# Optimization experiments

Hardware: AMD Instinct MI355X
Metric: run time of the kernel (lower is better)

Reference implementation:

```python
import jax, jax.numpy as jnp
import numpy as np

DEPTH = 4  # init kwarg 'depth'
H = 256   # init kwarg 'hidden_size'
ATOM_FDIM, BOND_FDIM = 35, 5


def _build_graph(rng, N, E):
    src = rng.integers(0, N, E).astype(np.int32)
    dst = rng.integers(0, N, E).astype(np.int32)
    # line graph (backtracking=False): lg edge e1 -> e2 iff dst[e1]==src[e2] and src[e1]!=dst[e2]
    indeg = np.bincount(dst, minlength=N)
    idx_sorted = np.argsort(dst, kind='stable')          # edge ids grouped by dst node
    ptr = np.concatenate([[0], np.cumsum(indeg)]).astype(np.int64)
    counts = indeg[src]                                   # in-edges of src[e] feed edge e
    total = int(counts.sum())
    lg_dst = np.repeat(np.arange(E, dtype=np.int64), counts)
    cum = np.cumsum(counts) - counts
    within = np.arange(total) - np.repeat(cum, counts)
    lg_src = idx_sorted[np.repeat(ptr[src], counts) + within]
    keep = src[lg_src] != dst[lg_dst]                     # drop backtracking pairs
    return src, dst, lg_src[keep].astype(np.int32), lg_dst[keep].astype(np.int32)


def setup_inputs() -> dict:
    rng = np.random.default_rng(0)
    N, E, Et, K, G = 50000, 200000, 100000, 50000, 2000
    src, dst, lg_src, lg_dst = _build_graph(rng, N, E)
    graph_ids = ((np.arange(N, dtype=np.int64) * G) // N).astype(np.int32)
    f32 = lambda *s: rng.standard_normal(s).astype(np.float32)
    return {
        'x_nodes': jnp.asarray(f32(N, ATOM_FDIM)),
        'x_edges': jnp.asarray(rng.random((E, BOND_FDIM)).astype(np.float32)),
        'tree_m': jnp.asarray(f32(Et, H) * 0.1),
        'W_i': jnp.asarray(f32(ATOM_FDIM + BOND_FDIM, H) * 0.05),
        'W_h': jnp.asarray(f32(H, H) * 0.05),
        'W_o': jnp.asarray(f32(ATOM_FDIM + H, H) * 0.05),
        'b_o': jnp.asarray(f32(H) * 0.05),
        'edge_src': jnp.asarray(src),
        'edge_dst': jnp.asarray(dst),
        'lg_src': jnp.asarray(lg_src),
        'lg_dst': jnp.asarray(lg_dst),
        'tgt_nodes': jnp.asarray(rng.integers(0, N, K).astype(np.int32)),
        'tree_eid': jnp.asarray(rng.integers(0, Et, K).astype(np.int32)),
        'graph_ids': jnp.asarray(graph_ids),
        'n_graphs': G,
    }


def reference(x_nodes, x_edges, tree_m, W_i, W_h, W_o, b_o,
              edge_src, edge_dst, lg_src, lg_dst, tgt_nodes, tree_eid,
              graph_ids, n_graphs):
    N = x_nodes.shape[0]
    E = x_edges.shape[0]
    # edge input features: [src atom feats | bond feats] @ W_i (no bias)
    msg_input = jnp.concatenate([x_nodes[edge_src], x_edges], axis=1) @ W_i  # [E,H]
    msg = jax.nn.relu(msg_input)
    # tree message alignment: scatter-add tree edge messages onto cand nodes
    node_alpha = jnp.zeros((N, msg.shape[1]), msg.dtype).at[tgt_nodes].add(tree_m[tree_eid])
    edge_alpha = node_alpha[edge_src]  # apply_edges: alpha = src alpha
    # loopy BP over the line graph
    for _ in range(DEPTH - 1):
        accum = jax.ops.segment_sum(msg[lg_src], lg_dst, num_segments=E)  # [E,H]
        msg = jax.nn.relu(msg_input + (accum + edge_alpha) @ W_h)
    # gather: m = sum of incoming edge messages per node
    m = jax.ops.segment_sum(msg, edge_dst, num_segments=N)  # [N,H]
    h = jax.nn.relu(jnp.concatenate([x_nodes, m + node_alpha], axis=1) @ W_o + b_o)
    # mean_nodes per candidate graph
    sums = jax.ops.segment_sum(h, graph_ids, num_segments=n_graphs)
    cnt = jax.ops.segment_sum(jnp.ones((N, 1), h.dtype), graph_ids, num_segments=n_graphs)
    return sums / jnp.maximum(cnt, 1.0)
```

## Files before the change

### kernel.cpp

```cpp
#include <hip/hip_runtime.h>
#include <stdint.h>

typedef unsigned short u16;
typedef __attribute__((ext_vector_type(8))) short bf16x8;
typedef __attribute__((ext_vector_type(4))) float f32x4;

#define HD 256
#define AST 264
#define CORR_CAP 2048

static __device__ __forceinline__ float b2f(u16 x){
  union{float f; unsigned u;} v; v.u = ((unsigned)x)<<16; return v.f;
}
static __device__ __forceinline__ u16 f2b(float f){
  union{float f; unsigned u;} v; v.f = f;
  unsigned r = v.u + 0x7fffu + ((v.u>>16)&1u);
  return (u16)(r>>16);
}
static __device__ __forceinline__ void racc2(float* a, uint2 iv, uint2 vv){
  float t0 = b2f((u16)iv.x)       + b2f((u16)vv.x);
  float t1 = b2f((u16)(iv.x>>16)) + b2f((u16)(vv.x>>16));
  float t2 = b2f((u16)iv.y)       + b2f((u16)vv.y);
  float t3 = b2f((u16)(iv.y>>16)) + b2f((u16)(vv.y>>16));
  a[0] += t0>0.f?t0:0.f; a[1] += t1>0.f?t1:0.f;
  a[2] += t2>0.f?t2:0.f; a[3] += t3>0.f?t3:0.f;
}
static __device__ __forceinline__ void racc1(float* a, uint2 iv){
  float t0 = b2f((u16)iv.x), t1 = b2f((u16)(iv.x>>16));
  float t2 = b2f((u16)iv.y), t3 = b2f((u16)(iv.y>>16));
  a[0] += t0>0.f?t0:0.f; a[1] += t1>0.f?t1:0.f;
  a[2] += t2>0.f?t2:0.f; a[3] += t3>0.f?t3:0.f;
}

__global__ void k_zero_int(int* __restrict__ p, int n){
  int i = blockIdx.x*256 + threadIdx.x;
  if (i < n) p[i] = 0;
}

__global__ void k_hist(const int* __restrict__ key, int* __restrict__ deg, int n){
  int i = blockIdx.x*256 + threadIdx.x;
  if (i < n) atomicAdd(&deg[key[i]], 1);
}

__global__ void k_scan_p1(const int* __restrict__ deg, int n, int* __restrict__ bsum){
  int i = blockIdx.x*256 + threadIdx.x;
  int v = (i < n) ? deg[i] : 0;
  #pragma unroll
  for (int o=32; o>0; o>>=1) v += __shfl_down(v, o);
  __shared__ int w[4];
  if ((threadIdx.x&63)==0) w[threadIdx.x>>6] = v;
  __syncthreads();
  if (threadIdx.x==0) bsum[blockIdx.x] = w[0]+w[1]+w[2]+w[3];
}
__global__ __launch_bounds__(1024) void k_scan_p2(int* __restrict__ bsum, int nb,
                                                  int* __restrict__ total_dst){
  __shared__ int sm[1024];
// ... 14 lines not shown
  int t = threadIdx.x;
  int i = blockIdx.x*256 + t;
  int v = (i < n) ? deg[i] : 0;
  __shared__ int sm[256];
  sm[t] = v; __syncthreads();
  for (int o=1; o<256; o<<=1){
    int u = (t>=o) ? sm[t-o] : 0;
    __syncthreads();
    sm[t] += u;
    __syncthreads();
  }
  int ex = sm[t] - v + bsum[blockIdx.x];
  if (i < n){ start[i] = ex; cursor[i] = ex; }
}

__global__ void k_fill(const int* __restrict__ key, const int* __restrict__ val,
                       int* __restrict__ cursor, int* __restrict__ bucket, int n){
  int i = blockIdx.x*256 + threadIdx.x;
  if (i >= n) return;
  int pos = atomicAdd(&cursor[key[i]], 1);
  bucket[pos] = val ? val[i] : i;
}

__global__ void k_permarr(const int* __restrict__ perm, const int* __restrict__ esrc,
                          const int* __restrict__ edst, int* __restrict__ esrc_p,
                          int* __restrict__ edst_p, int E){
  int e = blockIdx.x*256 + threadIdx.x;
  if (e >= E) return;
  int o = perm[e];
  esrc_p[e] = esrc[o];
  edst_p[e] = edst[o];
}

__global__ void k_xep(const float* __restrict__ xe, const int* __restrict__ perm,
                      float* __restrict__ xep, int E){
  int e = blockIdx.x*256 + threadIdx.x;
  if (e >= E) return;
  int o = perm[e];
  #pragma unroll
  for (int k=0;k<5;k++) xep[(size_t)e*5+k] = xe[(size_t)o*5+k];
}

__global__ void k_xnf(const float* __restrict__ xn, u16* __restrict__ xnf, int N){
  int g = blockIdx.x*256 + threadIdx.x;
  int v2 = g >> 6, c = g & 63;
  if (v2 >= N) return;
  float v = (c < 35) ? xn[(size_t)v2*35 + c] : 0.f;
  xnf[g] = f2b(v);
}

__global__ void k_alpha_gather(const float* __restrict__ tree_m, const int* __restrict__ start,
                               const int* __restrict__ bucket, u16* __restrict__ alpha16, int N){
  int v = (int)(((long long)blockIdx.x*blockDim.x + threadIdx.x)>>6);
  int l = threadIdx.x & 63;
  if (v >= N) return;
  int s = start[v], e2 = start[v+1];
  float a0=0.f,a1=0.f,a2=0.f,a3=0.f;
  for (int j=s;j<e2;j++){
    float4 tv = *(const float4*)(tree_m + (size_t)bucket[j]*HD + l*4);
    a0 += tv.x; a1 += tv.y; a2 += tv.z; a3 += tv.w;
  }
  ushort4 o; o.x=f2b(a0); o.y=f2b(a1); o.z=f2b(a2); o.w=f2b(a3);
  *(ushort4*)(alpha16 + (size_t)v*HD + l*4) = o;
}

__global__ void k_prep_frag(const float* __restrict__ W, int k0, int kmax, int nks,
                            u16* __restrict__ out){
  int g = blockIdx.x*256 + threadIdx.x;
  if (g >= nks*16*512) return;
  int i = g & 7, l = (g>>3)&63, t = g>>9;
  int nj = t & 15, ks = t >> 4;
  int n = nj*16 + (l&15);
  int k = ks*32 + (l>>4)*8 + i;
  float v = (k < kmax) ? W[(size_t)(k0+k)*HD + n] : 0.f;
  out[g] = f2b(v);
}

__global__ __launch_bounds__(512, 4) void k_pr_gemm(
    const u16* __restrict__ featA, const u16* __restrict__ BTf,
    u16* __restrict__ out16, int M)
{
  const int tid = threadIdx.x;
  const int w = tid>>6, l = tid&63;
  const int lr = l&15, lq = l>>4;
  const int nrb = (M+15)>>4;
  bf16x8 B0[2], B1[2];
  #pragma unroll
  for (int ks=0; ks<2; ks++){
    B0[ks] = *(const bf16x8*)(BTf + (size_t)((ks*16 + w*2  )*512) + l*8);
    B1[ks] = *(const bf16x8*)(BTf + (size_t)((ks*16 + w*2+1)*512) + l*8);
  }
  const int c0 = w*32 + lr, c1 = w*32 + 16 + lr;
  for (int rb = blockIdx.x; rb < nrb; rb += gridDim.x){
    int r = rb*16 + lr; int rc = min(r, M-1);
    const u16* fr = featA + (size_t)rc*64 + lq*8;
    bf16x8 a0 = *(const bf16x8*)(fr);
    bf16x8 a1 = *(const bf16x8*)(fr + 32);
    f32x4 acc0 = (f32x4){0.f,0.f,0.f,0.f};
    f32x4 acc1 = (f32x4){0.f,0.f,0.f,0.f};
    acc0 = __builtin_amdgcn_mfma_f32_16x16x32_bf16(a0, B0[0], acc0, 0,0,0);
    acc0 = __builtin_amdgcn_mfma_f32_16x16x32_bf16(a1, B0[1], acc0, 0,0,0);
    acc1 = __builtin_amdgcn_mfma_f32_16x16x32_bf16(a0, B1[0], acc1, 0,0,0);
    acc1 = __builtin_amdgcn_mfma_f32_16x16x32_bf16(a1, B1[1], acc1, 0,0,0);
    #pragma unroll
    for (int reg=0; reg<4; reg++){
      int gm = rb*16 + lq*4 + reg;
      if (gm < M){
        out16[(size_t)gm*HD + c0] = f2b(acc0[reg]);
        out16[(size_t)gm*HD + c1] = f2b(acc1[reg]);
      }
    }
  }
}

__global__ __launch_bounds__(256, 8) void k_build_I(
    const u16* __restrict__ P, const float* __restrict__ xep,
    const int* __restrict__ esrc_p, const float* __restrict__ Wi,
    u16* __restrict__ I, int E)
{
  const int l = threadIdx.x & 63;
  const int wid = (blockIdx.x*256 + threadIdx.x) >> 6;
  const int nw = gridDim.x*4;
  float wq[5][4];
  #pragma unroll
// ... 4 lines not shown
  for (int e = wid; e < E; e += nw){
    int s = esrc_p[e];
    const float* xp = xep + (size_t)e*5;
    float x0=xp[0], x1=xp[1], x2=xp[2], x3=xp[3], x4=xp[4];
    uint2 uv = *(const uint2*)(P + (size_t)s*HD + l*4);
    float v[4] = { b2f((u16)uv.x), b2f((u16)(uv.x>>16)),
                   b2f((u16)uv.y), b2f((u16)(uv.y>>16)) };
    #pragma unroll
    for (int j=0;j<4;j++)
      v[j] += x0*wq[0][j] + x1*wq[1][j] + x2*wq[2][j] + x3*wq[3][j] + x4*wq[4][j];
    ushort4 o; o.x=f2b(v[0]); o.y=f2b(v[1]); o.z=f2b(v[2]); o.w=f2b(v[3]);
    *(ushort4*)(I + (size_t)e*HD + l*4) = o;
  }
}

__global__ void k_pairs(const int* __restrict__ esrc_p, const int* __restrict__ edst_p,
                        const int* __restrict__ start_d,
                        int* __restrict__ npairs, int2* __restrict__ pairs, int E){
  int e = blockIdx.x*256 + threadIdx.x;
  if (e >= E) return;
  int u = esrc_p[e], v = edst_p[e];
  int s = start_d[u], t = start_d[u+1];
  for (int ep=s; ep<t; ep++){
    if (esrc_p[ep] == v){
      int pos = atomicAdd(npairs, 1);
      if (pos < CORR_CAP) pairs[pos] = (int2){e, ep};
    }
  }
}

__global__ void k_msgA0(const u16* __restrict__ I, const int2* __restrict__ pairs,
                        const int* __restrict__ npairs_p, float* __restrict__ msgA){
  int np = *npairs_p; if (np > CORR_CAP) np = CORR_CAP;
  int t = threadIdx.x;
  for (int p = blockIdx.x; p < np; p += gridDim.x){
    int ep = pairs[p].y;
    float v = b2f(I[(size_t)ep*HD + t]);
    msgA[(size_t)p*HD + t] = v > 0.f ? v : 0.f;
  }
}

__global__ __launch_bounds__(512, 4) void k_bp(
    const u16* __restrict__ I, const u16* __restrict__ Vprev,
    const u16* __restrict__ alpha16, const int* __restrict__ start_d,
    const int* __restrict__ esrc_p, const u16* __restrict__ BTf,
    const u16* __restrict__ Radd, const float* __restrict__ bias,
    u16* __restrict__ Sout, u16* __restrict__ Vout, float* __restrict__ hout,
    int N, int mode)
{
  __shared__ u16 A_lds[16][AST];
  const int tid = threadIdx.x;
  const int w = tid>>6, l = tid&63;
  const int lr = l&15, lq = l>>4;
  const int ngrp = (N+15)>>4;

  bf16x8 B0[8], B1[8];
  #pragma unroll
  for (int ks=0; ks<8; ks++){
    B0[ks] = *(const bf16x8*)(BTf + (size_t)((ks*16 + w*2  )*512) + l*8);
    B1[ks] = *(const bf16x8*)(BTf + (size_t)((ks*16 + w*2+1)*512) + l*8);
  }
  const int c0 = w*32 + lr, c1 = w*32 + 16 + lr;
  float b0 = 0.f, b1 = 0.f;
  if (mode == 1){ b0 = bias[c0]; b1 = bias[c1]; }

  for (int grp = blockIdx.x; grp < ngrp; grp += gridDim.x){
    const int vb = grp*16;
    #pragma unroll
    for (int hh=0; hh<2; hh++){
      int v = vb + w*2 + hh;
      float a[4] = {0.f,0.f,0.f,0.f};
      if (v < N){
        uint2 av = *(const uint2*)(alpha16 + (size_t)v*HD + l*4);
        a[0]=b2f((u16)av.x); a[1]=b2f((u16)(av.x>>16));
        a[2]=b2f((u16)av.y); a[3]=b2f((u16)(av.y>>16));
        int s = start_d[v], e2 = start_d[v+1];
        int cnt = e2 - s;
        const u16* Ir = I + (size_t)s*HD + l*4;
        if (Vprev){
          const int* sp = esrc_p + s;
          int j = 0;
          for (; j+2 <= cnt; j+=2){
            int s0 = sp[j], s1 = sp[j+1];
            uint2 i0 = *(const uint2*)(Ir);
            uint2 i1 = *(const uint2*)(Ir + HD);
            uint2 v0 = *(const uint2*)(Vprev + (size_t)s0*HD + l*4);
            uint2 v1 = *(const uint2*)(Vprev + (size_t)s1*HD + l*4);
            Ir += 2*HD;
            racc2(a, i0, v0); racc2(a, i1, v1);
          }
          if (j < cnt){
            int s0 = sp[j];
            uint2 i0 = *(const uint2*)(Ir);
            uint2 v0 = *(const uint2*)(Vprev + (size_t)s0*HD + l*4);
            racc2(a, i0, v0);
          }
        } else {
          int j = 0;
          for (; j+2 <= cnt; j+=2){
            uint2 i0 = *(const uint2*)(Ir);
            uint2 i1 = *(const uint2*)(Ir + HD);
            Ir += 2*HD;
            racc1(a, i0); racc1(a, i1);
          }
          if (j < cnt) racc1(a, *(const uint2*)(Ir));
        }
      }
      ushort4 o; o.x=f2b(a[0]); o.y=f2b(a[1]); o.z=f2b(a[2]); o.w=f2b(a[3]);
      if (v < N) *(ushort4*)(Sout + (size_t)v*HD + l*4) = o;
      *(ushort4*)&A_lds[w*2+hh][l*4] = o;
    }
    __syncthreads();
    f32x4 acc0 = (f32x4){0.f,0.f,0.f,0.f};
    f32x4 acc1 = (f32x4){0.f,0.f,0.f,0.f};
    const u16* Ar = &A_lds[lr][0];
    #pragma unroll
    for (int ks=0; ks<8; ks++){
      bf16x8 af = *(const bf16x8*)(Ar + ks*32 + lq*8);
      acc0 = __builtin_amdgcn_mfma_f32_16x16x32_bf16(af, B0[ks], acc0, 0,0,0);
      acc1 = __builtin_amdgcn_mfma_f32_16x16x32_bf16(af, B1[ks], acc1, 0,0,0);
    }
    #pragma unroll
    for (int reg=0; reg<4; reg++){
      int gm = vb + lq*4 + reg;
      if (gm < N){
        if (mode == 1){
          float v0 = acc0[reg] + b2f(Radd[(size_t)gm*HD + c0]) + b0;
          float v1 = acc1[reg] + b2f(Radd[(size_t)gm*HD + c1]) + b1;
          hout[(size_t)gm*HD + c0] = v0 > 0.f ? v0 : 0.f;
          hout[(size_t)gm*HD + c1] = v1 > 0.f ? v1 : 0.f;
        } else {
          Vout[(size_t)gm*HD + c0] = f2b(acc0[reg]);
          Vout[(size_t)gm*HD + c1] = f2b(acc1[reg]);
        }
      }
    }
    __syncthreads();
  }
}

__global__ __launch_bounds__(256) void k_corr1(
    const u16* __restrict__ I, const u16* __restrict__ Vprev,
    const int* __restrict__ esrc_p,
    const int2* __restrict__ pairs, const int* __restrict__ npairs_p,
    const float* __restrict__ Wh, const float* __restrict__ msgA,
    float* __restrict__ newA, float* __restrict__ deltaS)
{
  int np = *npairs_p; if (np > CORR_CAP) np = CORR_CAP;
// ... 14 lines not shown
      float a0=0.f,a1=0.f,a2=0.f,a3=0.f;
      for (int k=0;k<HD;k+=4){
        a0 += cs[k]  *Wh[(size_t)k*HD+t];
        a1 += cs[k+1]*Wh[(size_t)(k+1)*HD+t];
        a2 += cs[k+2]*Wh[(size_t)(k+2)*HD+t];
        a3 += cs[k+3]*Wh[(size_t)(k+3)*HD+t];
      }
      float corr = (a0+a1)+(a2+a3);
      int u = esrc_p[e];
      float base = b2f(I[(size_t)e*HD + t]) + b2f(Vprev[(size_t)u*HD + t]);
      float mn = base > 0.f ? base : 0.f;
      float bt = base - corr;
      float mt = bt > 0.f ? bt : 0.f;
      deltaS[(size_t)p*HD + t] = mt - mn;
      for (int q=0;q<np;q++) if (pairs[q].y == e) newA[(size_t)q*HD + t] = mt;
    }
  }
}

__global__ __launch_bounds__(256, 1) void k_corr2(
    const int2* __restrict__ pairs, const int* __restrict__ npairs_p,
    const int* __restrict__ edst_p, const float* __restrict__ deltaS,
    float* __restrict__ msgA, const float* __restrict__ newA,
    u16* __restrict__ Scur)
{
  int np = *npairs_p; if (np > CORR_CAP) np = CORR_CAP;
  int t = threadIdx.x;
  for (int p=0; p<np; p++){
    msgA[(size_t)p*HD + t] = newA[(size_t)p*HD + t];
    int e = pairs[p].x;
    bool first = true;
    for (int q=0;q<p;q++) if (pairs[q].x == e){ first=false; break; }
    if (first){
      int dv = edst_p[e];
      u16* sp = Scur + (size_t)dv*HD + t;
      *sp = f2b(b2f(*sp) + deltaS[(size_t)p*HD + t]);
    }
    __syncthreads();
  }
}

__global__ __launch_bounds__(256) void k_corr3(
    const int2* __restrict__ pairs, const int* __restrict__ npairs_p,
    const int* __restrict__ edst_p, const u16* __restrict__ Scur,
    const float* __restrict__ Wh, const float* __restrict__ Wob,
    const u16* __restrict__ Radd, const float* __restrict__ bias,
    u16* __restrict__ Vcur, float* __restrict__ hout, int isfinal)
{
  int np = *npairs_p; if (np > CORR_CAP) np = CORR_CAP;
  int t = threadIdx.x;
  __shared__ float sa[HD];
  for (int p = blockIdx.x; p < np; p += gridDim.x){
    int dv = edst_p[pairs[p].x];
    bool first = true;
    for (int q=0;q<p;q++) if (edst_p[pairs[q].x] == dv){ first=false; break; }
    __syncthreads();
    if (first) sa[t] = b2f(Scur[(size_t)dv*HD + t]);
    __syncthreads();
    if (first){
      const float* W = isfinal ? Wob : Wh;
      float a0=0.f,a1=0.f,a2=0.f,a3=0.f;
      for (int k=0;k<HD;k+=4){
        a0 += sa[k]  *W[(size_t)k*HD+t];
        a1 += sa[k+1]*W[(size_t)(k+1)*HD+t];
        a2 += sa[k+2]*W[(size_t)(k+2)*HD+t];
        a3 += sa[k+3]*W[(size_t)(k+3)*HD+t];
      }
      float acc = (a0+a1)+(a2+a3);
      if (isfinal){
        float hv = acc + b2f(Radd[(size_t)dv*HD + t]) + bias[t];
        hout[(size_t)dv*HD + t] = hv > 0.f ? hv : 0.f;
      } else {
        Vcur[(size_t)dv*HD + t] = f2b(acc);
      }
    }
  }
}

__global__ void k_graph_mean(const float* __restrict__ h, const int* __restrict__ gid,
                             int N, int G, float* __restrict__ out){
  int g = (int)(((long long)blockIdx.x*blockDim.x + threadIdx.x)>>6);
  int l = threadIdx.x & 63;
  if (g >= G) return;
  int lo=0, hi=N;
  while (lo<hi){ int mid=(lo+hi)>>1; if (gid[mid] < g) lo=mid+1; else hi=mid; }
  int b = lo;
  hi = N;
  while (lo<hi){ int mid=(lo+hi)>>1; if (gid[mid] < g+1) lo=mid+1; else hi=mid; }
  int e2 = lo;
// ... 16 lines not shown
  const float* tree_m  = (const float*)d_in[2];
  const float* W_i     = (const float*)d_in[3];
  const float* W_h     = (const float*)d_in[4];
  const float* W_o     = (const float*)d_in[5];
  const float* b_o     = (const float*)d_in[6];
  const int* edge_src = (const int*)d_in[7];
  const int* edge_dst = (const int*)d_in[8];
  const int* tgt      = (const int*)d_in[11];
  const int* teid     = (const int*)d_in[12];
  const int* gid      = (const int*)d_in[13];

  const int N = in_sizes[0]/35;
  const int E = in_sizes[1]/5;
  const int K = in_sizes[11];
  const int G = out_size/HD;

  char* wsb = (char*)d_ws;
  auto align256 = [](size_t x){ return (x + 255) & ~(size_t)255; };
  size_t oI      = 0;
  size_t oSa     = oI      + align256((size_t)E*HD*2);
  size_t oVa     = oSa     + align256((size_t)N*HD*2);
  size_t oP      = oVa     + align256((size_t)N*HD*2);
  size_t oVb     = oP      + align256((size_t)N*HD*2);
  size_t oR      = oVb     + align256((size_t)N*HD*2);
  size_t oAlpha  = oR      + align256((size_t)N*HD*2);
  size_t oXnf    = oAlpha  + align256((size_t)N*HD*2);
  size_t oXep    = oXnf    + align256((size_t)N*64*2);
  size_t oBTP    = oXep    + align256((size_t)E*5*4);
  size_t oBTWh   = oBTP    + align256((size_t)2*16*512*2);
  size_t oBTRa   = oBTWh   + align256((size_t)8*16*512*2);
  size_t oBTWob  = oBTRa   + align256((size_t)2*16*512*2);
  size_t oDegD   = oBTWob  + align256((size_t)8*16*512*2);
  size_t oStartD = oDegD   + align256((size_t)(N+1)*4);
  size_t oCurD   = oStartD + align256((size_t)(N+1)*4);
  size_t oPerm   = oCurD   + align256((size_t)N*4);
  size_t oEsrcP  = oPerm   + align256((size_t)E*4);
  size_t oEdstP  = oEsrcP  + align256((size_t)E*4);
  size_t oDegT   = oEdstP  + align256((size_t)E*4);
  size_t oStartT = oDegT   + align256((size_t)N*4);
  size_t oCurT   = oStartT + align256((size_t)(N+1)*4);
  size_t oBukT   = oCurT   + align256((size_t)N*4);
  size_t oBsum   = oBukT   + align256((size_t)K*4);
  size_t oPairs  = oBsum   + align256((size_t)1024*4);
  size_t oMsgA   = oPairs  + align256((size_t)CORR_CAP*8);
  size_t oNewA   = oMsgA   + align256((size_t)CORR_CAP*HD*4);
  size_t oDeltaS = oNewA   + align256((size_t)CORR_CAP*HD*4);

  u16*   I       = (u16*)(wsb + oI);
  u16*   Sa      = (u16*)(wsb + oSa);
  u16*   Va      = (u16*)(wsb + oVa);
  u16*   P       = (u16*)(wsb + oP);
  u16*   Vb      = (u16*)(wsb + oVb);
  u16*   R       = (u16*)(wsb + oR);
  u16*   alpha16 = (u16*)(wsb + oAlpha);
  u16*   xnf     = (u16*)(wsb + oXnf);
  float* xep     = (float*)(wsb + oXep);
  u16*   BT_P    = (u16*)(wsb + oBTP);
  u16*   BT_Wh   = (u16*)(wsb + oBTWh);
  u16*   BT_Ra   = (u16*)(wsb + oBTRa);
  u16*   BT_Wob  = (u16*)(wsb + oBTWob);
  int*   deg_d   = (int*)(wsb + oDegD);
  int*   npairs  = deg_d + N;
  int*   start_d = (int*)(wsb + oStartD);
  int*   cur_d   = (int*)(wsb + oCurD);
  int*   perm    = (int*)(wsb + oPerm);
  int*   esrc_p  = (int*)(wsb + oEsrcP);
  int*   edst_p  = (int*)(wsb + oEdstP);
  int*   deg_t   = (int*)(wsb + oDegT);
  int*   start_t = (int*)(wsb + oStartT);
  int*   cur_t   = (int*)(wsb + oCurT);
  int*   buk_t   = (int*)(wsb + oBukT);
  int*   bsum    = (int*)(wsb + oBsum);
  int2*  pairs   = (int2*)(wsb + oPairs);
  float* msgA    = (float*)(wsb + oMsgA);
  float* newA    = (float*)(wsb + oNewA);
  float* deltaS  = (float*)(wsb + oDeltaS);
  float* hbuf    = (float*)(wsb + oP);

  const int egrid256 = (E+255)/256;
  const int kgrid256 = (K+255)/256;
  const int ngrid256 = (N+255)/256;
  const int nbN      = (N+255)/256;

  k_prep_frag<<<64,  256, 0, stream>>>(W_i, 0, 35, 2, BT_P);
  k_prep_frag<<<256, 256, 0, stream>>>(W_h, 0, 256, 8, BT_Wh);
  k_prep_frag<<<64,  256, 0, stream>>>(W_o, 0, 35, 2, BT_Ra);
  k_prep_frag<<<256, 256, 0, stream>>>(W_o, 35, 256, 8, BT_Wob);

  k_zero_int<<<(N+1+255)/256, 256, 0, stream>>>(deg_d, N+1);
  k_hist<<<egrid256, 256, 0, stream>>>(edge_dst, deg_d, E);
  k_scan_p1<<<nbN, 256, 0, stream>>>(deg_d, N, bsum);
  k_scan_p2<<<1, 1024, 0, stream>>>(bsum, nbN, start_d + N);
  k_scan_p3<<<nbN, 256, 0, stream>>>(deg_d, bsum, N, start_d, cur_d);
  k_fill<<<egrid256, 256, 0, stream>>>(edge_dst, (const int*)0, cur_d, perm, E);
  k_permarr<<<egrid256, 256, 0, stream>>>(perm, edge_src, edge_dst, esrc_p, edst_p, E);
  k_xep<<<egrid256, 256, 0, stream>>>(x_edges, perm, xep, E);
  k_xnf<<<((size_t)N*64+255)/256, 256, 0, stream>>>(x_nodes, xnf, N);

  k_zero_int<<<ngrid256, 256, 0, stream>>>(deg_t, N);
  k_hist<<<kgrid256, 256, 0, stream>>>(tgt, deg_t, K);
  k_scan_p1<<<nbN, 256, 0, stream>>>(deg_t, N, bsum);
  k_scan_p2<<<1, 1024, 0, stream>>>(bsum, nbN, start_t + N);
  k_scan_p3<<<nbN, 256, 0, stream>>>(deg_t, bsum, N, start_t, cur_t);
  k_fill<<<kgrid256, 256, 0, stream>>>(tgt, teid, cur_t, buk_t, K);
  k_alpha_gather<<<(N+3)/4, 256, 0, stream>>>(tree_m, start_t, buk_t, alpha16, N);

  k_pairs<<<egrid256, 256, 0, stream>>>(esrc_p, edst_p, start_d, npairs, pairs, E);

  k_pr_gemm<<<512, 512, 0, stream>>>(xnf, BT_P, P, N);
  k_pr_gemm<<<512, 512, 0, stream>>>(xnf, BT_Ra, R, N);

  k_build_I<<<2048, 256, 0, stream>>>(P, xep, esrc_p, W_i, I, E);
  k_msgA0<<<64, 256, 0, stream>>>(I, pairs, npairs, msgA);

  const float* Wob = W_o + 35*HD;

  k_bp<<<1024, 512, 0, stream>>>(I, (const u16*)0, alpha16, start_d, esrc_p, BT_Wh,
                                 (const u16*)0, (const float*)0, Sa, Va, (float*)0, N, 0);
  k_bp<<<1024, 512, 0, stream>>>(I, Va, alpha16, start_d, esrc_p, BT_Wh,
                                 (const u16*)0, (const float*)0, Sa, Vb, (float*)0, N, 0);
  k_corr1<<<64, 256, 0, stream>>>(I, Va, esrc_p, pairs, npairs, W_h, msgA, newA, deltaS);
  k_corr2<<<1, 256, 0, stream>>>(pairs, npairs, edst_p, deltaS, msgA, newA, Sa);
  k_corr3<<<64, 256, 0, stream>>>(pairs, npairs, edst_p, Sa, W_h, Wob,
                                  (const u16*)0, (const float*)0, Vb, (float*)0, 0);
  k_bp<<<1024, 512, 0, stream>>>(I, Vb, alpha16, start_d, esrc_p, BT_Wh,
                                 (const u16*)0, (const float*)0, Sa, Va, (float*)0, N, 0);
  k_corr1<<<64, 256, 0, stream>>>(I, Vb, esrc_p, pairs, npairs, W_h, msgA, newA, deltaS);
  k_corr2<<<1, 256, 0, stream>>>(pairs, npairs, edst_p, deltaS, msgA, newA, Sa);
  k_corr3<<<64, 256, 0, stream>>>(pairs, npairs, edst_p, Sa, W_h, Wob,
                                  (const u16*)0, (const float*)0, Va, (float*)0, 0);
  k_bp<<<1024, 512, 0, stream>>>(I, Va, alpha16, start_d, esrc_p, BT_Wob,
                                 R, b_o, Sa, (u16*)0, hbuf, N, 1);
  k_corr1<<<64, 256, 0, stream>>>(I, Va, esrc_p, pairs, npairs, W_h, msgA, newA, deltaS);
  k_corr2<<<1, 256, 0, stream>>>(pairs, npairs, edst_p, deltaS, msgA, newA, Sa);
  k_corr3<<<64, 256, 0, stream>>>(pairs, npairs, edst_p, Sa, W_h, Wob,
                                  R, b_o, (u16*)0, hbuf, 1);

  k_graph_mean<<<(G+3)/4, 256, 0, stream>>>(hbuf, gid, N, G, (float*)d_out);
}
```

Measured before the change: 674.9 us.

## Fuse setup kernels, merge CSR builds, enlarge BP node groups, add correction kernel

Folds the four weight-fragment preps, zeroing and node-feature conversion into one launch. The tree-target and edge-destination CSR builds now share one histogram/scan/fill pass, and the alpha gather and pair search run in one kernel. The two small projection GEMMs are fused into one. The BP kernel processes 64 nodes per block instead of 16, loads source indices cooperatively with shuffles, and drops the intermediate Sout write in non-final iterations. A new k_corrV replaces the corr2/corr3 pair for the middle iterations. Together these reduce launch count and redundant traffic, at the cost of more LDS per block and possibly lower occupancy in k_bp.

```diff
diff --git a/kernel.cpp b/kernel.cpp
--- a/kernel.cpp
+++ b/kernel.cpp
@@ -7,6 +7,7 @@
 
 #define HD 256
 #define AST 264
+#define GRP 64
 #define CORR_CAP 2048
 
 static __device__ __forceinline__ float b2f(u16 x){
@@ -32,14 +33,56 @@
   a[2] += t2>0.f?t2:0.f; a[3] += t3>0.f?t3:0.f;
 }
 
-__global__ void k_zero_int(int* __restrict__ p, int n){
-  int i = blockIdx.x*256 + threadIdx.x;
-  if (i < n) p[i] = 0;
-}
-
-__global__ void k_hist(const int* __restrict__ key, int* __restrict__ deg, int n){
-  int i = blockIdx.x*256 + threadIdx.x;
-  if (i < n) atomicAdd(&deg[key[i]], 1);
+static __device__ __forceinline__ void prep_frag_body(const float* __restrict__ W,
+    int k0, int kmax, u16* __restrict__ out, int lb, int tid){
+  int g = lb*256 + tid;
+  int i = g & 7, l = (g>>3)&63, t = g>>9;
+  int nj = t & 15, ks = t >> 4;
+  int n = nj*16 + (l&15);
+  int k = ks*32 + (l>>4)*8 + i;
+  float v = (k < kmax) ? W[(size_t)(k0+k)*HD + n] : 0.f;
+  out[g] = f2b(v);
+}
+__global__ void k_prep_all(const float* __restrict__ Wi, const float* __restrict__ Wh,
+                           const float* __restrict__ Wo, const float* __restrict__ xn,
+                           u16* __restrict__ BT_P, u16* __restrict__ BT_Wh,
+                           u16* __restrict__ BT_Ra, u16* __restrict__ BT_Wob,
+                           u16* __restrict__ xnf, int* __restrict__ deg2,
+                           int N, int zb){
+  int b = blockIdx.x, tid = threadIdx.x;
+  if (b < 64){ prep_frag_body(Wi, 0, 35, BT_P, b, tid); return; }
+  b -= 64;
+  if (b < 256){ prep_frag_body(Wh, 0, 256, BT_Wh, b, tid); return; }
+  b -= 256;
+  if (b < 64){ prep_frag_body(Wo, 0, 35, BT_Ra, b, tid); return; }
+  b -= 64;
+  if (b < 256){ prep_frag_body(Wo, 35, 256, BT_Wob, b, tid); return; }
+  b -= 256;
+  if (b < zb){
+    int i = b*256 + tid;
+    if (i < 2*N+1) deg2[i] = 0;
+    return;
+  }
+  b -= zb;
+  {
+    long long g = (long long)b*256 + tid;
+    int v2 = (int)(g >> 6), c = (int)(g & 63);
+    if (v2 >= N) return;
+    float v = (c < 35) ? xn[(size_t)v2*35 + c] : 0.f;
+    xnf[g] = f2b(v);
+  }
+}
+
+__global__ void k_hist2(const int* __restrict__ tgt, const int* __restrict__ edst,
+                        int* __restrict__ deg2, int K, int E, int N, int kgrid){
+  int b = blockIdx.x;
+  if (b < kgrid){
+    int i = b*256 + threadIdx.x;
+    if (i < K) atomicAdd(&deg2[tgt[i]], 1);
+  } else {
+    int i = (b-kgrid)*256 + threadIdx.x;
+    if (i < E) atomicAdd(&deg2[N + edst[i]], 1);
+  }
 }
 
 __global__ void k_scan_p1(const int* __restrict__ deg, int n, int* __restrict__ bsum){
@@ -84,100 +127,110 @@
   if (i < n){ start[i] = ex; cursor[i] = ex; }
 }
 
-__global__ void k_fill(const int* __restrict__ key, const int* __restrict__ val,
-                       int* __restrict__ cursor, int* __restrict__ bucket, int n){
-  int i = blockIdx.x*256 + threadIdx.x;
-  if (i >= n) return;
-  int pos = atomicAdd(&cursor[key[i]], 1);
-  bucket[pos] = val ? val[i] : i;
-}
-
-__global__ void k_permarr(const int* __restrict__ perm, const int* __restrict__ esrc,
-                          const int* __restrict__ edst, int* __restrict__ esrc_p,
-                          int* __restrict__ edst_p, int E){
+__global__ void k_fill2(const int* __restrict__ tgt, const int* __restrict__ teid,
+                        const int* __restrict__ edst, int* __restrict__ cursor2,
+                        int* __restrict__ bucket2, int K, int E, int N, int kgrid){
+  int b = blockIdx.x;
+  if (b < kgrid){
+    int i = b*256 + threadIdx.x;
+    if (i >= K) return;
+    int pos = atomicAdd(&cursor2[tgt[i]], 1);
+    bucket2[pos] = teid[i];
+  } else {
+    int e = (b-kgrid)*256 + threadIdx.x;
+    if (e >= E) return;
+    int pos = atomicAdd(&cursor2[N + edst[e]], 1);
+    bucket2[pos] = e;
+  }
+}
+
+__global__ void k_perm_xep(const int* __restrict__ bucket2, int K,
+                           const int* __restrict__ esrc, const int* __restrict__ edst,
+                           const float* __restrict__ xe,
+                           int* __restrict__ esrc_p, int* __restrict__ edst_p,
+                           float* __restrict__ xep, int E){
   int e = blockIdx.x*256 + threadIdx.x;
   if (e >= E) return;
-  int o = perm[e];
+  int o = bucket2[K + e];
   esrc_p[e] = esrc[o];
   edst_p[e] = edst[o];
-}
-
-__global__ void k_xep(const float* __restrict__ xe, const int* __restrict__ perm,
-                      float* __restrict__ xep, int E){
-  int e = blockIdx.x*256 + threadIdx.x;
-  if (e >= E) return;
-  int o = perm[e];
   #pragma unroll
   for (int k=0;k<5;k++) xep[(size_t)e*5+k] = xe[(size_t)o*5+k];
 }
 
-__global__ void k_xnf(const float* __restrict__ xn, u16* __restrict__ xnf, int N){
-  int g = blockIdx.x*256 + threadIdx.x;
-  int v2 = g >> 6, c = g & 63;
-  if (v2 >= N) return;
-  float v = (c < 35) ? xn[(size_t)v2*35 + c] : 0.f;
-  xnf[g] = f2b(v);
-}
-
-__global__ void k_alpha_gather(const float* __restrict__ tree_m, const int* __restrict__ start,
-                               const int* __restrict__ bucket, u16* __restrict__ alpha16, int N){
-  int v = (int)(((long long)blockIdx.x*blockDim.x + threadIdx.x)>>6);
-  int l = threadIdx.x & 63;
-  if (v >= N) return;
-  int s = start[v], e2 = start[v+1];
-  float a0=0.f,a1=0.f,a2=0.f,a3=0.f;
-  for (int j=s;j<e2;j++){
-    float4 tv = *(const float4*)(tree_m + (size_t)bucket[j]*HD + l*4);
-    a0 += tv.x; a1 += tv.y; a2 += tv.z; a3 += tv.w;
-  }
-  ushort4 o; o.x=f2b(a0); o.y=f2b(a1); o.z=f2b(a2); o.w=f2b(a3);
-  *(ushort4*)(alpha16 + (size_t)v*HD + l*4) = o;
-}
-
-__global__ void k_prep_frag(const float* __restrict__ W, int k0, int kmax, int nks,
-                            u16* __restrict__ out){
-  int g = blockIdx.x*256 + threadIdx.x;
-  if (g >= nks*16*512) return;
-  int i = g & 7, l = (g>>3)&63, t = g>>9;
-  int nj = t & 15, ks = t >> 4;
-  int n = nj*16 + (l&15);
-  int k = ks*32 + (l>>4)*8 + i;
-  float v = (k < kmax) ? W[(size_t)(k0+k)*HD + n] : 0.f;
-  out[g] = f2b(v);
-}
-
-__global__ __launch_bounds__(512, 4) void k_pr_gemm(
-    const u16* __restrict__ featA, const u16* __restrict__ BTf,
-    u16* __restrict__ out16, int M)
+__global__ void k_alpha_pairs(const float* __restrict__ tree_m,
+                              const int* __restrict__ start2, const int* __restrict__ bucket2,
+                              u16* __restrict__ alpha16,
+                              const int* __restrict__ esrc_p, const int* __restrict__ edst_p,
+                              int* __restrict__ npairs, int2* __restrict__ pairs,
+                              int N, int E, int K, int agrid){
+  int b = blockIdx.x;
+  if (b < agrid){
+    int v = (int)(((long long)b*256 + threadIdx.x)>>6);
+    int l = threadIdx.x & 63;
+    if (v >= N) return;
+    int s = start2[v], e2 = start2[v+1];
+    float a0=0.f,a1=0.f,a2=0.f,a3=0.f;
+    for (int j=s;j<e2;j++){
+      float4 tv = *(const float4*)(tree_m + (size_t)bucket2[j]*HD + l*4);
+      a0 += tv.x; a1 += tv.y; a2 += tv.z; a3 += tv.w;
+    }
+    ushort4 o; o.x=f2b(a0); o.y=f2b(a1); o.z=f2b(a2); o.w=f2b(a3);
+    *(ushort4*)(alpha16 + (size_t)v*HD + l*4) = o;
+  } else {
+    int e = (b-agrid)*256 + threadIdx.x;
+    if (e >= E) return;
+    int u = esrc_p[e], v = edst_p[e];
+    int s = start2[N+u] - K, t = start2[N+u+1] - K;
+    for (int ep=s; ep<t; ep++){
+      if (esrc_p[ep] == v){
+        int pos = atomicAdd(npairs, 1);
+        if (pos < CORR_CAP) pairs[pos] = (int2){e, ep};
+      }
+    }
+  }
+}
+
+__global__ __launch_bounds__(512, 4) void k_pr2(
+    const u16* __restrict__ xnf, const u16* __restrict__ BT_P,
+    const u16* __restrict__ BT_Ra, u16* __restrict__ P, u16* __restrict__ R, int M)
 {
   const int tid = threadIdx.x;
   const int w = tid>>6, l = tid&63;
   const int lr = l&15, lq = l>>4;
   const int nrb = (M+15)>>4;
-  bf16x8 B0[2], B1[2];
+  bf16x8 BP0[2], BP1[2], BR0[2], BR1[2];
   #pragma unroll
   for (int ks=0; ks<2; ks++){
-    B0[ks] = *(const bf16x8*)(BTf + (size_t)((ks*16 + w*2  )*512) + l*8);
-    B1[ks] = *(const bf16x8*)(BTf + (size_t)((ks*16 + w*2+1)*512) + l*8);
+    BP0[ks] = *(const bf16x8*)(BT_P  + (size_t)((ks*16 + w*2  )*512) + l*8);
+    BP1[ks] = *(const bf16x8*)(BT_P  + (size_t)((ks*16 + w*2+1)*512) + l*8);
+    BR0[ks] = *(const bf16x8*)(BT_Ra + (size_t)((ks*16 + w*2  )*512) + l*8);
+    BR1[ks] = *(const bf16x8*)(BT_Ra + (size_t)((ks*16 + w*2+1)*512) + l*8);
   }
   const int c0 = w*32 + lr, c1 = w*32 + 16 + lr;
   for (int rb = blockIdx.x; rb < nrb; rb += gridDim.x){
     int r = rb*16 + lr; int rc = min(r, M-1);
-    const u16* fr = featA + (size_t)rc*64 + lq*8;
+    const u16* fr = xnf + (size_t)rc*64 + lq*8;
     bf16x8 a0 = *(const bf16x8*)(fr);
     bf16x8 a1 = *(const bf16x8*)(fr + 32);
-    f32x4 acc0 = (f32x4){0.f,0.f,0.f,0.f};
-    f32x4 acc1 = (f32x4){0.f,0.f,0.f,0.f};
-    acc0 = __builtin_amdgcn_mfma_f32_16x16x32_bf16(a0, B0[0], acc0, 0,0,0);
-    acc0 = __builtin_amdgcn_mfma_f32_16x16x32_bf16(a1, B0[1], acc0, 0,0,0);
-    acc1 = __builtin_amdgcn_mfma_f32_16x16x32_bf16(a0, B1[0], acc1, 0,0,0);
-    acc1 = __builtin_amdgcn_mfma_f32_16x16x32_bf16(a1, B1[1], acc1, 0,0,0);
+    f32x4 p0={0.f,0.f,0.f,0.f}, p1={0.f,0.f,0.f,0.f};
+    f32x4 r0={0.f,0.f,0.f,0.f}, r1={0.f,0.f,0.f,0.f};
+    p0 = __builtin_amdgcn_mfma_f32_16x16x32_bf16(a0, BP0[0], p0, 0,0,0);
+    p0 = __builtin_amdgcn_mfma_f32_16x16x32_bf16(a1, BP0[1], p0, 0,0,0);
+    p1 = __builtin_amdgcn_mfma_f32_16x16x32_bf16(a0, BP1[0], p1, 0,0,0);
+    p1 = __builtin_amdgcn_mfma_f32_16x16x32_bf16(a1, BP1[1], p1, 0,0,0);
+    r0 = __builtin_amdgcn_mfma_f32_16x16x32_bf16(a0, BR0[0], r0, 0,0,0);
+    r0 = __builtin_amdgcn_mfma_f32_16x16x32_bf16(a1, BR0[1], r0, 0,0,0);
+    r1 = __builtin_amdgcn_mfma_f32_16x16x32_bf16(a0, BR1[0], r1, 0,0,0);
+    r1 = __builtin_amdgcn_mfma_f32_16x16x32_bf16(a1, BR1[1], r1, 0,0,0);
     #pragma unroll
     for (int reg=0; reg<4; reg++){
       int gm = rb*16 + lq*4 + reg;
       if (gm < M){
-        out16[(size_t)gm*HD + c0] = f2b(acc0[reg]);
-        out16[(size_t)gm*HD + c1] = f2b(acc1[reg]);
+        P[(size_t)gm*HD + c0] = f2b(p0[reg]);
+        P[(size_t)gm*HD + c1] = f2b(p1[reg]);
+        R[(size_t)gm*HD + c0] = f2b(r0[reg]);
+        R[(size_t)gm*HD + c1] = f2b(r1[reg]);
       }
     }
   }
@@ -212,21 +265,6 @@
   }
 }
 
-__global__ void k_pairs(const int* __restrict__ esrc_p, const int* __restrict__ edst_p,
-                        const int* __restrict__ start_d,
-                        int* __restrict__ npairs, int2* __restrict__ pairs, int E){
-  int e = blockIdx.x*256 + threadIdx.x;
-  if (e >= E) return;
-  int u = esrc_p[e], v = edst_p[e];
-  int s = start_d[u], t = start_d[u+1];
-  for (int ep=s; ep<t; ep++){
-    if (esrc_p[ep] == v){
-      int pos = atomicAdd(npairs, 1);
-      if (pos < CORR_CAP) pairs[pos] = (int2){e, ep};
-    }
-  }
-}
-
 __global__ void k_msgA0(const u16* __restrict__ I, const int2* __restrict__ pairs,
                         const int* __restrict__ npairs_p, float* __restrict__ msgA){
   int np = *npairs_p; if (np > CORR_CAP) np = CORR_CAP;
@@ -238,19 +276,19 @@
   }
 }
 
-__global__ __launch_bounds__(512, 4) void k_bp(
+__global__ __launch_bounds__(512, 8) void k_bp(
     const u16* __restrict__ I, const u16* __restrict__ Vprev,
-    const u16* __restrict__ alpha16, const int* __restrict__ start_d,
+    const u16* __restrict__ alpha16, const int* __restrict__ start_d, int KBIAS,
     const int* __restrict__ esrc_p, const u16* __restrict__ BTf,
     const u16* __restrict__ Radd, const float* __restrict__ bias,
     u16* __restrict__ Sout, u16* __restrict__ Vout, float* __restrict__ hout,
     int N, int mode)
 {
-  __shared__ u16 A_lds[16][AST];
+  __shared__ u16 A_lds[GRP][AST];
   const int tid = threadIdx.x;
   const int w = tid>>6, l = tid&63;
   const int lr = l&15, lq = l>>4;
-  const int ngrp = (N+15)>>4;
+  const int ngrp = (N+GRP-1)/GRP;
 
   bf16x8 B0[8], B1[8];
   #pragma unroll
@@ -263,73 +301,79 @@
   if (mode == 1){ b0 = bias[c0]; b1 = bias[c1]; }
 
   for (int grp = blockIdx.x; grp < ngrp; grp += gridDim.x){
-    const int vb = grp*16;
-    #pragma unroll
-    for (int hh=0; hh<2; hh++){
-      int v = vb + w*2 + hh;
+    const int vb = grp*GRP;
+    for (int hh=0; hh<8; hh++){
+      int v = vb + w*8 + hh;
       float a[4] = {0.f,0.f,0.f,0.f};
       if (v < N){
         uint2 av = *(const uint2*)(alpha16 + (size_t)v*HD + l*4);
         a[0]=b2f((u16)av.x); a[1]=b2f((u16)(av.x>>16));
         a[2]=b2f((u16)av.y); a[3]=b2f((u16)(av.y>>16));
-        int s = start_d[v], e2 = start_d[v+1];
+        int s = start_d[v] - KBIAS, e2 = start_d[v+1] - KBIAS;
         int cnt = e2 - s;
-        const u16* Ir = I + (size_t)s*HD + l*4;
+        const u16* Ir0 = I + (size_t)s*HD + l*4;
         if (Vprev){
           const int* sp = esrc_p + s;
-          int j = 0;
-          for (; j+2 <= cnt; j+=2){
-            int s0 = sp[j], s1 = sp[j+1];
-            uint2 i0 = *(const uint2*)(Ir);
-            uint2 i1 = *(const uint2*)(Ir + HD);
-            uint2 v0 = *(const uint2*)(Vprev + (size_t)s0*HD + l*4);
-            uint2 v1 = *(const uint2*)(Vprev + (size_t)s1*HD + l*4);
-            Ir += 2*HD;
-            racc2(a, i0, v0); racc2(a, i1, v1);
-          }
-          if (j < cnt){
-            int s0 = sp[j];
-            uint2 i0 = *(const uint2*)(Ir);
-            uint2 v0 = *(const uint2*)(Vprev + (size_t)s0*HD + l*4);
-            racc2(a, i0, v0);
+          int done = 0;
+          while (done < cnt){
+            int m = min(64, cnt - done);
+            int idx = (l < m) ? sp[done + l] : 0;
+            int j = 0;
+            for (; j+2 <= m; j+=2){
+              int s0 = __shfl(idx, j), s1 = __shfl(idx, j+1);
+              uint2 i0 = *(const uint2*)(Ir0 + (size_t)(done+j  )*HD);
+              uint2 i1 = *(const uint2*)(Ir0 + (size_t)(done+j+1)*HD);
+              uint2 v0 = *(const uint2*)(Vprev + (size_t)s0*HD + l*4);
+              uint2 v1 = *(const uint2*)(Vprev + (size_t)s1*HD + l*4);
+              racc2(a, i0, v0); racc2(a, i1, v1);
+            }
+            if (j < m){
+              int s0 = __shfl(idx, j);
+              uint2 i0 = *(const uint2*)(Ir0 + (size_t)(done+j)*HD);
+              uint2 v0 = *(const uint2*)(Vprev + (size_t)s0*HD + l*4);
+              racc2(a, i0, v0);
+            }
+            done += m;
           }
         } else {
           int j = 0;
           for (; j+2 <= cnt; j+=2){
-            uint2 i0 = *(const uint2*)(Ir);
-            uint2 i1 = *(const uint2*)(Ir + HD);
-            Ir += 2*HD;
+            uint2 i0 = *(const uint2*)(Ir0 + (size_t)j*HD);
+            uint2 i1 = *(const uint2*)(Ir0 + (size_t)(j+1)*HD);
             racc1(a, i0); racc1(a, i1);
           }
-          if (j < cnt) racc1(a, *(const uint2*)(Ir));
+          if (j < cnt) racc1(a, *(const uint2*)(Ir0 + (size_t)j*HD));
         }
       }
       ushort4 o; o.x=f2b(a[0]); o.y=f2b(a[1]); o.z=f2b(a[2]); o.w=f2b(a[3]);
-      if (v < N) *(ushort4*)(Sout + (size_t)v*HD + l*4) = o;
-      *(ushort4*)&A_lds[w*2+hh][l*4] = o;
-    }
-    __syncthreads();
-    f32x4 acc0 = (f32x4){0.f,0.f,0.f,0.f};
-    f32x4 acc1 = (f32x4){0.f,0.f,0.f,0.f};
-    const u16* Ar = &A_lds[lr][0];
+      if (v < N && Sout) *(ushort4*)(Sout + (size_t)v*HD + l*4) = o;
+      *(ushort4*)&A_lds[w*8+hh][l*4] = o;
+    }
+    __syncthreads();
     #pragma unroll
-    for (int ks=0; ks<8; ks++){
-      bf16x8 af = *(const bf16x8*)(Ar + ks*32 + lq*8);
-      acc0 = __builtin_amdgcn_mfma_f32_16x16x32_bf16(af, B0[ks], acc0, 0,0,0);
-      acc1 = __builtin_amdgcn_mfma_f32_16x16x32_bf16(af, B1[ks], acc1, 0,0,0);
-    }
-    #pragma unroll
-    for (int reg=0; reg<4; reg++){
-      int gm = vb + lq*4 + reg;
-      if (gm < N){
-        if (mode == 1){
-          float v0 = acc0[reg] + b2f(Radd[(size_t)gm*HD + c0]) + b0;
-          float v1 = acc1[reg] + b2f(Radd[(size_t)gm*HD + c1]) + b1;
-          hout[(size_t)gm*HD + c0] = v0 > 0.f ? v0 : 0.f;
-          hout[(size_t)gm*HD + c1] = v1 > 0.f ? v1 : 0.f;
-        } else {
-          Vout[(size_t)gm*HD + c0] = f2b(acc0[reg]);
-          Vout[(size_t)gm*HD + c1] = f2b(acc1[reg]);
+    for (int t4=0; t4<4; t4++){
+      f32x4 acc0 = (f32x4){0.f,0.f,0.f,0.f};
+      f32x4 acc1 = (f32x4){0.f,0.f,0.f,0.f};
+      const u16* Ar = &A_lds[t4*16 + lr][0];
+      #pragma unroll
+      for (int ks=0; ks<8; ks++){
+        bf16x8 af = *(const bf16x8*)(Ar + ks*32 + lq*8);
+        acc0 = __builtin_amdgcn_mfma_f32_16x16x32_bf16(af, B0[ks], acc0, 0,0,0);
+        acc1 = __builtin_amdgcn_mfma_f32_16x16x32_bf16(af, B1[ks], acc1, 0,0,0);
+      }
+      #pragma unroll
+      for (int reg=0; reg<4; reg++){
+        int gm = vb + t4*16 + lq*4 + reg;
+        if (gm < N){
+          if (mode == 1){
+            float v0 = acc0[reg] + b2f(Radd[(size_t)gm*HD + c0]) + b0;
+            float v1 = acc1[reg] + b2f(Radd[(size_t)gm*HD + c1]) + b1;
+            hout[(size_t)gm*HD + c0] = v0 > 0.f ? v0 : 0.f;
+            hout[(size_t)gm*HD + c1] = v1 > 0.f ? v1 : 0.f;
+          } else {
+            Vout[(size_t)gm*HD + c0] = f2b(acc0[reg]);
+            Vout[(size_t)gm*HD + c1] = f2b(acc1[reg]);
+          }
         }
       }
     }
@@ -374,6 +418,48 @@
       float mt = bt > 0.f ? bt : 0.f;
       deltaS[(size_t)p*HD + t] = mt - mn;
       for (int q=0;q<np;q++) if (pairs[q].y == e) newA[(size_t)q*HD + t] = mt;
+    }
+  }
+}
+
+__global__ __launch_bounds__(256) void k_corrV(
+    const int2* __restrict__ pairs, const int* __restrict__ npairs_p,
+    const int* __restrict__ edst_p, const float* __restrict__ deltaS,
+    float* __restrict__ msgA, const float* __restrict__ newA,
+    const float* __restrict__ Wh, u16* __restrict__ Vcur)
+{
+  int np = *npairs_p; if (np > CORR_CAP) np = CORR_CAP;
+  int t = threadIdx.x;
+  __shared__ float ds[HD];
+  for (int p = blockIdx.x; p < np; p += gridDim.x)
+    msgA[(size_t)p*HD + t] = newA[(size_t)p*HD + t];
+  for (int p = blockIdx.x; p < np; p += gridDim.x){
+    int dv = edst_p[pairs[p].x];
+    bool firstdv = true;
+    for (int q=0;q<p;q++) if (edst_p[pairs[q].x] == dv){ firstdv=false; break; }
+    __syncthreads();
+    if (firstdv){
+      float d = 0.f;
+      for (int q=p;q<np;q++){
+        if (edst_p[pairs[q].x] != dv) continue;
+        bool fe = true;
+        for (int r=0;r<q;r++) if (pairs[r].x == pairs[q].x){ fe=false; break; }
+        if (fe) d += deltaS[(size_t)q*HD + t];
+      }
+      ds[t] = d;
+    }
+    __syncthreads();
+    if (firstdv){
+      float a0=0.f,a1=0.f,a2=0.f,a3=0.f;
+      for (int k=0;k<HD;k+=4){
+        a0 += ds[k]  *Wh[(size_t)k*HD+t];
+        a1 += ds[k+1]*Wh[(size_t)(k+1)*HD+t];
+        a2 += ds[k+2]*Wh[(size_t)(k+2)*HD+t];
+        a3 += ds[k+3]*Wh[(size_t)(k+3)*HD+t];
+      }
+      float dot = (a0+a1)+(a2+a3);
+      u16* vp = Vcur + (size_t)dv*HD + t;
+      *vp = f2b(b2f(*vp) + dot);
     }
   }
 }
@@ -403,9 +489,8 @@
 __global__ __launch_bounds__(256) void k_corr3(
     const int2* __restrict__ pairs, const int* __restrict__ npairs_p,
     const int* __restrict__ edst_p, const u16* __restrict__ Scur,
-    const float* __restrict__ Wh, const float* __restrict__ Wob,
-    const u16* __restrict__ Radd, const float* __restrict__ bias,
-    u16* __restrict__ Vcur, float* __restrict__ hout, int isfinal)
+    const float* __restrict__ Wob, const u16* __restrict__ Radd,
+    const float* __restrict__ bias, float* __restrict__ hout)
 {
   int np = *npairs_p; if (np > CORR_CAP) np = CORR_CAP;
   int t = threadIdx.x;
@@ -418,21 +503,16 @@
     if (first) sa[t] = b2f(Scur[(size_t)dv*HD + t]);
     __syncthreads();
     if (first){
-      const float* W = isfinal ? Wob : Wh;
       float a0=0.f,a1=0.f,a2=0.f,a3=0.f;
       for (int k=0;k<HD;k+=4){
-        a0 += sa[k]  *W[(size_t)k*HD+t];
-        a1 += sa[k+1]*W[(size_t)(k+1)*HD+t];
-        a2 += sa[k+2]*W[(size_t)(k+2)*HD+t];
-        a3 += sa[k+3]*W[(size_t)(k+3)*HD+t];
+        a0 += sa[k]  *Wob[(size_t)k*HD+t];
+        a1 += sa[k+1]*Wob[(size_t)(k+1)*HD+t];
+        a2 += sa[k+2]*Wob[(size_t)(k+2)*HD+t];
+        a3 += sa[k+3]*Wob[(size_t)(k+3)*HD+t];
       }
       float acc = (a0+a1)+(a2+a3);
-      if (isfinal){
-        float hv = acc + b2f(Radd[(size_t)dv*HD + t]) + bias[t];
-        hout[(size_t)dv*HD + t] = hv > 0.f ? hv : 0.f;
-      } else {
-        Vcur[(size_t)dv*HD + t] = f2b(acc);
-      }
+      float hv = acc + b2f(Radd[(size_t)dv*HD + t]) + bias[t];
+      hout[(size_t)dv*HD + t] = hv > 0.f ? hv : 0.f;
     }
   }
 }
@@ -479,6 +559,7 @@
   const int E = in_sizes[1]/5;
   const int K = in_sizes[11];
   const int G = out_size/HD;
+  const int N2 = 2*N;
 
   char* wsb = (char*)d_ws;
   auto align256 = [](size_t x){ return (x + 255) & ~(size_t)255; };
@@ -495,17 +576,13 @@
   size_t oBTWh   = oBTP    + align256((size_t)2*16*512*2);
   size_t oBTRa   = oBTWh   + align256((size_t)8*16*512*2);
   size_t oBTWob  = oBTRa   + align256((size_t)2*16*512*2);
-  size_t oDegD   = oBTWob  + align256((size_t)8*16*512*2);
-  size_t oStartD = oDegD   + align256((size_t)(N+1)*4);
-  size_t oCurD   = oStartD + align256((size_t)(N+1)*4);
-  size_t oPerm   = oCurD   + align256((size_t)N*4);
-  size_t oEsrcP  = oPerm   + align256((size_t)E*4);
+  size_t oDeg2   = oBTWob  + align256((size_t)8*16*512*2);
+  size_t oStart2 = oDeg2   + align256((size_t)(N2+1)*4);
+  size_t oCur2   = oStart2 + align256((size_t)(N2+1)*4);
+  size_t oBuk2   = oCur2   + align256((size_t)N2*4);
+  size_t oEsrcP  = oBuk2   + align256((size_t)(K+E)*4);
   size_t oEdstP  = oEsrcP  + align256((size_t)E*4);
-  size_t oDegT   = oEdstP  + align256((size_t)E*4);
-  size_t oStartT = oDegT   + align256((size_t)N*4);
-  size_t oCurT   = oStartT + align256((size_t)(N+1)*4);
-  size_t oBukT   = oCurT   + align256((size_t)N*4);
-  size_t oBsum   = oBukT   + align256((size_t)K*4);
+  size_t oBsum   = oEdstP  + align256((size_t)E*4);
   size_t oPairs  = oBsum   + align256((size_t)1024*4);
   size_t oMsgA   = oPairs  + align256((size_t)CORR_CAP*8);
   size_t oNewA   = oMsgA   + align256((size_t)CORR_CAP*HD*4);
@@ -524,17 +601,13 @@
   u16*   BT_Wh   = (u16*)(wsb + oBTWh);
   u16*   BT_Ra   = (u16*)(wsb + oBTRa);
   u16*   BT_Wob  = (u16*)(wsb + oBTWob);
-  int*   deg_d   = (int*)(wsb + oDegD);
-  int*   npairs  = deg_d + N;
-  int*   start_d = (int*)(wsb + oStartD);
-  int*   cur_d   = (int*)(wsb + oCurD);
-  int*   perm    = (int*)(wsb + oPerm);
+  int*   deg2    = (int*)(wsb + oDeg2);
+  int*   npairs  = deg2 + N2;
+  int*   start2  = (int*)(wsb + oStart2);
+  int*   cursor2 = (int*)(wsb + oCur2);
+  int*   bucket2 = (int*)(wsb + oBuk2);
   int*   esrc_p  = (int*)(wsb + oEsrcP);
   int*   edst_p  = (int*)(wsb + oEdstP);
-  int*   deg_t   = (int*)(wsb + oDegT);
-  int*   start_t = (int*)(wsb + oStartT);
-  int*   cur_t   = (int*)(wsb + oCurT);
-  int*   buk_t   = (int*)(wsb + oBukT);
   int*   bsum    = (int*)(wsb + oBsum);
   int2*  pairs   = (int2*)(wsb + oPairs);
   float* msgA    = (float*)(wsb + oMsgA);
@@ -544,62 +617,51 @@
 
   const int egrid256 = (E+255)/256;
   const int kgrid256 = (K+255)/256;
-  const int ngrid256 = (N+255)/256;
-  const int nbN      = (N+255)/256;
-
-  k_prep_frag<<<64,  256, 0, stream>>>(W_i, 0, 35, 2, BT_P);
-  k_prep_frag<<<256, 256, 0, stream>>>(W_h, 0, 256, 8, BT_Wh);
-  k_prep_frag<<<64,  256, 0, stream>>>(W_o, 0, 35, 2, BT_Ra);
-  k_prep_frag<<<256, 256, 0, stream>>>(W_o, 35, 256, 8, BT_Wob);
-
-  k_zero_int<<<(N+1+255)/256, 256, 0, stream>>>(deg_d, N+1);
-  k_hist<<<egrid256, 256, 0, stream>>>(edge_dst, deg_d, E);
-  k_scan_p1<<<nbN, 256, 0, stream>>>(deg_d, N, bsum);
-  k_scan_p2<<<1, 1024, 0, stream>>>(bsum, nbN, start_d + N);
-  k_scan_p3<<<nbN, 256, 0, stream>>>(deg_d, bsum, N, start_d, cur_d);
-  k_fill<<<egrid256, 256, 0, stream>>>(edge_dst, (const int*)0, cur_d, perm, E);
-  k_permarr<<<egrid256, 256, 0, stream>>>(perm, edge_src, edge_dst, esrc_p, edst_p, E);
-  k_xep<<<egrid256, 256, 0, stream>>>(x_edges, perm, xep, E);
-  k_xnf<<<((size_t)N*64+255)/256, 256, 0, stream>>>(x_nodes, xnf, N);
-
-  k_zero_int<<<ngrid256, 256, 0, stream>>>(deg_t, N);
-  k_hist<<<kgrid256, 256, 0, stream>>>(tgt, deg_t, K);
-  k_scan_p1<<<nbN, 256, 0, stream>>>(deg_t, N, bsum);
-  k_scan_p2<<<1, 1024, 0, stream>>>(bsum, nbN, start_t + N);
-  k_scan_p3<<<nbN, 256, 0, stream>>>(deg_t, bsum, N, start_t, cur_t);
-  k_fill<<<kgrid256, 256, 0, stream>>>(tgt, teid, cur_t, buk_t, K);
-  k_alpha_gather<<<(N+3)/4, 256, 0, stream>>>(tree_m, start_t, buk_t, alpha16, N);
-
-  k_pairs<<<egrid256, 256, 0, stream>>>(esrc_p, edst_p, start_d, npairs, pairs, E);
-
-  k_pr_gemm<<<512, 512, 0, stream>>>(xnf, BT_P, P, N);
-  k_pr_gemm<<<512, 512, 0, stream>>>(xnf, BT_Ra, R, N);
-
+  const int nb2      = (N2+255)/256;
+  const int zb       = (N2+1+255)/256;
+  const int xnfb     = (int)(((size_t)N*64+255)/256);
+  const int agrid    = (N+3)/4;
+  const int ngrp     = (N+GRP-1)/GRP;
+
+  k_prep_all<<<640+zb+xnfb, 256, 0, stream>>>(W_i, W_h, W_o, x_nodes,
+                                              BT_P, BT_Wh, BT_Ra, BT_Wob,
+                                              xnf, deg2, N, zb);
+  k_hist2<<<kgrid256+egrid256, 256, 0, stream>>>(tgt, edge_dst, deg2, K, E, N, kgrid256);
+  k_scan_p1<<<nb2, 256, 0, stream>>>(deg2, N2, bsum);
+  k_scan_p2<<<1, 1024, 0, stream>>>(bsum, nb2, start2 + N2);
+  k_scan_p3<<<nb2, 256, 0, stream>>>(deg2, bsum, N2, start2, cursor2);
+  k_fill2<<<kgrid256+egrid256, 256, 0, stream>>>(tgt, teid, edge_dst, cursor2, bucket2,
+                                                 K, E, N, kgrid256);
+  k_perm_xep<<<egrid256, 256, 0, stream>>>(bucket2, K, edge_src, edge_dst, x_edges,
+                                           esrc_p, edst_p, xep, E);
+  k_alpha_pairs<<<agrid+egrid256, 256, 0, stream>>>(tree_m, start2, bucket2, alpha16,
+                                                    esrc_p, edst_p, npairs, pairs,
+                                                    N, E, K, agrid);
+  k_pr2<<<512, 512, 0, stream>>>(xnf, BT_P, BT_Ra, P, R, N);
   k_build_I<<<2048, 256, 0, stream>>>(P, xep, esrc_p, W_i, I, E);
   k_msgA0<<<64, 256, 0, stream>>>(I, pairs, npairs, msgA);
 
   const float* Wob = W_o + 35*HD;
-
-  k_bp<<<1024, 512, 0, stream>>>(I, (const u16*)0, alpha16, start_d, esrc_p, BT_Wh,
-                                 (const u16*)0, (const float*)0, Sa, Va, (float*)0, N, 0);
-  k_bp<<<1024, 512, 0, stream>>>(I, Va, alpha16, start_d, esrc_p, BT_Wh,
-                                 (const u16*)0, (const float*)0, Sa, Vb, (float*)0, N, 0);
+  const int* start_d = start2 + N;
+
+  k_bp<<<ngrp, 512, 0, stream>>>(I, (const u16*)0, alpha16, start_d, K, esrc_p, BT_Wh,
+                                 (const u16*)0, (const float*)0,
+                                 (u16*)0, Va, (float*)0, N, 0);
+  k_bp<<<ngrp, 512, 0, stream>>>(I, Va, alpha16, start_d, K, esrc_p, BT_Wh,
+                                 (const u16*)0, (const float*)0,
+                                 (u16*)0, Vb, (float*)0, N, 0);
   k_corr1<<<64, 256, 0, stream>>>(I, Va, esrc_p, pairs, npairs, W_h, msgA, newA, deltaS);
-  k_corr2<<<1, 256, 0, stream>>>(pairs, npairs, edst_p, deltaS, msgA, newA, Sa);
-  k_corr3<<<64, 256, 0, stream>>>(pairs, npairs, edst_p, Sa, W_h, Wob,
-                                  (const u16*)0, (const float*)0, Vb, (float*)0, 0);
-  k_bp<<<1024, 512, 0, stream>>>(I, Vb, alpha16, start_d, esrc_p, BT_Wh,
-                                 (const u16*)0, (const float*)0, Sa, Va, (float*)0, N, 0);
+  k_corrV<<<64, 256, 0, stream>>>(pairs, npairs, edst_p, deltaS, msgA, newA, W_h, Vb);
+  k_bp<<<ngrp, 512, 0, stream>>>(I, Vb, alpha16, start_d, K, esrc_p, BT_Wh,
+                                 (const u16*)0, (const float*)0,
+                                 (u16*)0, Va, (float*)0, N, 0);
   k_corr1<<<64, 256, 0, stream>>>(I, Vb, esrc_p, pairs, npairs, W_h, msgA, newA, deltaS);
-  k_corr2<<<1, 256, 0, stream>>>(pairs, npairs, edst_p, deltaS, msgA, newA, Sa);
-  k_corr3<<<64, 256, 0, stream>>>(pairs, npairs, edst_p, Sa, W_h, Wob,
-                                  (const u16*)0, (const float*)0, Va, (float*)0, 0);
-  k_bp<<<1024, 512, 0, stream>>>(I, Va, alpha16, start_d, esrc_p, BT_Wob,
+  k_corrV<<<64, 256, 0, stream>>>(pairs, npairs, edst_p, deltaS, msgA, newA, W_h, Va);
+  k_bp<<<ngrp, 512, 0, stream>>>(I, Va, alpha16, start_d, K, esrc_p, BT_Wob,
                                  R, b_o, Sa, (u16*)0, hbuf, N, 1);
   k_corr1<<<64, 256, 0, stream>>>(I, Va, esrc_p, pairs, npairs, W_h, msgA, newA, deltaS);
   k_corr2<<<1, 256, 0, stream>>>(pairs, npairs, edst_p, deltaS, msgA, newA, Sa);
-  k_corr3<<<64, 256, 0, stream>>>(pairs, npairs, edst_p, Sa, W_h, Wob,
-                                  R, b_o, (u16*)0, hbuf, 1);
+  k_corr3<<<64, 256, 0, stream>>>(pairs, npairs, edst_p, Sa, Wob, R, b_o, hbuf);
 
   k_graph_mean<<<(G+3)/4, 256, 0, stream>>>(hbuf, gid, N, G, (float*)d_out);
 }
```

Result: slower. 994.5 us (+47.4%).
